# Kernel tuning notes

Hardware: AMD Instinct MI355X
Metric: run time of the kernel (lower is better)

Reference implementation:

```python
import jax, jax.numpy as jnp
import numpy as np

N_NODES = 100000
N_EDGES = 3200000
N_GRAPHS = 128


def setup_inputs() -> dict:
    key = jax.random.key(0)
    ks = jax.random.split(key, 16)
    x = jax.random.normal(ks[0], (N_NODES, 47), dtype=jnp.float32)
    edge_index = jax.random.randint(ks[1], (2, N_EDGES), 0, N_NODES, dtype=jnp.int32)
    batch = jnp.sort(jax.random.randint(ks[2], (N_NODES,), 0, N_GRAPHS, dtype=jnp.int32))

    def w(k, shape):
        fan_in = shape[0]
        return jax.random.normal(k, shape, dtype=jnp.float32) * (1.0 / np.sqrt(fan_in))

    return {
        "x": x, "edge_index": edge_index, "batch": batch,
        "W1": w(ks[3], (47, 64)), "b1": jnp.zeros((64,), jnp.float32),
        "W2": w(ks[4], (64, 32)), "b2": jnp.zeros((32,), jnp.float32),
        "A1": w(ks[5], (32, 32)), "c1": jnp.zeros((32,), jnp.float32),
        "A2": w(ks[6], (32, 16)), "c2": jnp.zeros((16,), jnp.float32),
        "A3": w(ks[7], (16, 8)),  "c3": jnp.zeros((8,), jnp.float32),
        "A4": w(ks[8], (8, 1)),   "c4": jnp.zeros((1,), jnp.float32),
    }


def _gcn_conv(x, W, b, src, dst):
    # PyG GCNConv: h = XW, then D^-1/2 (A+I) D^-1/2 aggregation, then + bias.
    h = x @ W  # [N, out]
    ones = jnp.ones(dst.shape[0], dtype=h.dtype)
    deg = jax.ops.segment_sum(ones, dst, num_segments=N_NODES)  # incl. self loops
    dinv = jnp.where(deg > 0, jax.lax.rsqrt(deg), 0.0)
    norm = dinv[src] * dinv[dst]  # [E_total]
    msg = h[src] * norm[:, None]  # gather + normalize
    out = jax.ops.segment_sum(msg, dst, num_segments=N_NODES)  # scatter-add
    return out + b


def reference(x, edge_index, batch, W1, b1, W2, b2, A1, c1, A2, c2, A3, c3, A4, c4):
    loops = jnp.arange(N_NODES, dtype=edge_index.dtype)
    src = jnp.concatenate([edge_index[0], loops])
    dst = jnp.concatenate([edge_index[1], loops])
    h = jax.nn.relu(_gcn_conv(x, W1, b1, src, dst))
    h = jax.nn.relu(_gcn_conv(h, W2, b2, src, dst))
    # dropout is identity in eval mode
    g = jax.ops.segment_sum(h, batch, num_segments=N_GRAPHS)  # global_add_pool [G,32]
    g = jax.nn.relu(g @ A1 + c1)
    g = jax.nn.relu(g @ A2 + c2)
    g = jax.nn.relu(g @ A3 + c3)
    return g @ A4 + c4  # [G, 1]
```

## Files before the change

kernel.cpp:

```cpp
#include <hip/hip_runtime.h>

#define N_NODES 100000
#define N_EDGES 3200000
#define N_GRAPHS 128

#define RSHIFT 8
#define NPR 256
#define R_RANGES ((N_NODES + NPR - 1) / NPR)
#define CAP 9472
#define C_CHUNKS 1024
#define EPC (N_EDGES / C_CHUNKS)
#define SRC_BITS 17

#define XPB 64
#define AXW 48

__device__ inline unsigned short f2bf(float f) {
    unsigned u = __float_as_uint(f);
    unsigned r = u + 0x7FFFu + ((u >> 16) & 1u);
    return (unsigned short)(r >> 16);
}
__device__ inline float bflo(unsigned u) { return __uint_as_float(u << 16); }
__device__ inline float bfhi(unsigned u) { return __uint_as_float(u & 0xFFFF0000u); }


__global__ __launch_bounds__(256) void padcvt_kernel(const float* __restrict__ x,
                                                     unsigned short* __restrict__ xpb,
                                                     int* __restrict__ range_next) {
    if (blockIdx.x < 2) {
        int i = blockIdx.x * 256 + threadIdx.x;
        if (i < R_RANGES) range_next[i] = i * CAP;
    }
    int idx = blockIdx.x * 256 + threadIdx.x;
    if (idx >= N_NODES * XPB) return;
    int n = idx >> 6;
    int c = idx & 63;
    float v = (c < 47) ? x[n * 47 + c] : 0.f;
    xpb[idx] = f2bf(v);
}


__global__ __launch_bounds__(256) void partition_kernel(const int* __restrict__ src,
                                                        const int* __restrict__ dst,
                                                        int* __restrict__ range_next,
                                                        int* __restrict__ bucket) {
    __shared__ int cntL[R_RANGES];
    __shared__ int baseL[R_RANGES];
    const int t = threadIdx.x, b = blockIdx.x;
    const int e0 = b * EPC, e1 = e0 + EPC;
    for (int i = t; i < R_RANGES; i += 256) cntL[i] = 0;
    __syncthreads();
    for (int e = e0 + t; e < e1; e += 256) atomicAdd(&cntL[dst[e] >> RSHIFT], 1);
    __syncthreads();
    for (int i = t; i < R_RANGES; i += 256) {
        int c = cntL[i];
        baseL[i] = (c > 0) ? atomicAdd(&range_next[i], c) : 0;
        cntL[i] = 0;
    }
    __syncthreads();
    for (int e = e0 + t; e < e1; e += 256) {
        int d = dst[e];
        int s = src[e];
        int r = d >> RSHIFT;
        int p = baseL[r] + atomicAdd(&cntL[r], 1);
        if (p < (r + 1) * CAP)
            bucket[p] = ((d & (NPR - 1)) << SRC_BITS) | s;
    }
}


__global__ __launch_bounds__(256) void build_kernel(const int* __restrict__ bucket,
                                                    const int* __restrict__ range_next,
                                                    int* __restrict__ row_ptr,
                                                    int* __restrict__ row_cnt,
                                                    float* __restrict__ dinv,
                                                    int* __restrict__ csr_src) {
    __shared__ int sE[CAP];
    __shared__ int degs[NPR];
    __shared__ int part[256];
    const int t = threadIdx.x, r = blockIdx.x;
    const int base_node = r * NPR;
    const int seg0 = r * CAP;
    int m = range_next[r] - seg0;
    if (m > CAP) m = CAP;
    for (int i = t; i < m; i += 256) sE[i] = bucket[seg0 + i];
    degs[t] = 0;
    __syncthreads();
    for (int i = t; i < m; i += 256) atomicAdd(&degs[sE[i] >> SRC_BITS], 1);
    __syncthreads();
    int d = degs[t];
    part[t] = d;
    __syncthreads();
    for (int dd = 1; dd < 256; dd <<= 1) {
        int tv = (t >= dd) ? part[t - dd] : 0;
        __syncthreads();
        part[t] += tv;
        __syncthreads();
    }
    int ex = part[t] - d;
    int node = base_node + t;
    if (node < N_NODES) {
        row_ptr[node] = seg0 + ex;
        row_cnt[node] = d;
        dinv[node] = rsqrtf((float)(d + 1));
    }
    degs[t] = ex;
    __syncthreads();
    for (int i = t; i < m; i += 256) {
        int p = sE[i];
        int pos = atomicAdd(&degs[p >> SRC_BITS], 1);
        csr_src[seg0 + pos] = p & ((1 << SRC_BITS) - 1);
    }
}


__global__ __launch_bounds__(256) void wprep_kernel(const int* __restrict__ csr_src,
                                                    const int* __restrict__ range_next,
                                                    const float* __restrict__ dinv,
                                                    float* __restrict__ csr_w) {
    const int t = threadIdx.x, r = blockIdx.x;
    const int seg0 = r * CAP;
    int m = range_next[r] - seg0;
    if (m > CAP) m = CAP;
    for (int i = t; i < m; i += 256) {
        csr_w[seg0 + i] = dinv[csr_src[seg0 + i]];
    }
}


__global__ __launch_bounds__(256) void aggX_kernel(const unsigned short* __restrict__ xpb,
                                                   const float* __restrict__ dinv,
                                                   const int* __restrict__ row_ptr,
                                                   const int* __restrict__ row_cnt,
                                                   const int* __restrict__ csr_src,
                                                   const float* __restrict__ csr_w,
                                                   unsigned short* __restrict__ aggxb) {
    const int tid = threadIdx.x;
    const int n = blockIdx.x * 4 + (tid >> 6);
    if (n >= N_NODES) return;
    const int l = tid & 63;
    const int eo = l >> 3;
    const int cg = l & 7;
    const float dn = dinv[n];

    float acc[8] = {0.f, 0.f, 0.f, 0.f, 0.f, 0.f, 0.f, 0.f};
    if (eo == 0) {
        uint4 q = *(const uint4*)(xpb + (size_t)n * XPB + cg * 8);
        float w = dn * dn;
        acc[0] = bflo(q.x) * w; acc[1] = bfhi(q.x) * w;
        acc[2] = bflo(q.y) * w; acc[3] = bfhi(q.y) * w;
        acc[4] = bflo(q.z) * w; acc[5] = bfhi(q.z) * w;
        acc[6] = bflo(q.w) * w; acc[7] = bfhi(q.w) * w;
    }
    const int st = row_ptr[n];
    const int cnt = row_cnt[n];
    int k = eo;
    for (; k + 8 < cnt; k += 16) {
        int s0 = csr_src[st + k];
        int s1 = csr_src[st + k + 8];
        float w0 = csr_w[st + k] * dn;
        float w1 = csr_w[st + k + 8] * dn;
        uint4 q0 = *(const uint4*)(xpb + (size_t)s0 * XPB + cg * 8);
        uint4 q1 = *(const uint4*)(xpb + (size_t)s1 * XPB + cg * 8);
        acc[0] = fmaf(bflo(q0.x), w0, acc[0]); acc[1] = fmaf(bfhi(q0.x), w0, acc[1]);
        acc[2] = fmaf(bflo(q0.y), w0, acc[2]); acc[3] = fmaf(bfhi(q0.y), w0, acc[3]);
        acc[4] = fmaf(bflo(q0.z), w0, acc[4]); acc[5] = fmaf(bfhi(q0.z), w0, acc[5]);
        acc[6] = fmaf(bflo(q0.w), w0, acc[6]); acc[7] = fmaf(bfhi(q0.w), w0, acc[7]);
        acc[0] = fmaf(bflo(q1.x), w1, acc[0]); acc[1] = fmaf(bfhi(q1.x), w1, acc[1]);
        acc[2] = fmaf(bflo(q1.y), w1, acc[2]); acc[3] = fmaf(bfhi(q1.y), w1, acc[3]);
        acc[4] = fmaf(bflo(q1.z), w1, acc[4]); acc[5] = fmaf(bfhi(q1.z), w1, acc[5]);
        acc[6] = fmaf(bflo(q1.w), w1, acc[6]); acc[7] = fmaf(bfhi(q1.w), w1, acc[7]);
    }
    if (k < cnt) {
        int s0 = csr_src[st + k];
        float w0 = csr_w[st + k] * dn;
        uint4 q0 = *(const uint4*)(xpb + (size_t)s0 * XPB + cg * 8);
        acc[0] = fmaf(bflo(q0.x), w0, acc[0]); acc[1] = fmaf(bfhi(q0.x), w0, acc[1]);
        acc[2] = fmaf(bflo(q0.y), w0, acc[2]); acc[3] = fmaf(bfhi(q0.y), w0, acc[3]);
        acc[4] = fmaf(bflo(q0.z), w0, acc[4]); acc[5] = fmaf(bfhi(q0.z), w0, acc[5]);
        acc[6] = fmaf(bflo(q0.w), w0, acc[6]); acc[7] = fmaf(bfhi(q0.w), w0, acc[7]);
    }
#pragma unroll
    for (int off = 8; off <= 32; off <<= 1) {
#pragma unroll
        for (int j = 0; j < 8; ++j) acc[j] += __shfl_xor(acc[j], off);
    }
    if (eo == 0 && cg < 6) {
        uint4 o;
        o.x = ((unsigned)f2bf(acc[1]) << 16) | f2bf(acc[0]);
        o.y = ((unsigned)f2bf(acc[3]) << 16) | f2bf(acc[2]);
        o.z = ((unsigned)f2bf(acc[5]) << 16) | f2bf(acc[4]);
        o.w = ((unsigned)f2bf(acc[7]) << 16) | f2bf(acc[6]);
        *(uint4*)(aggxb + (size_t)n * AXW + cg * 8) = o;
    }
}


#define FGW1 52
#define FGW2 68

__global__ __launch_bounds__(256) void fusedgemm_kernel(const unsigned short* __restrict__ aggxb,
                                                        const float* __restrict__ W1,
                                                        const float* __restrict__ b1,
                                                        const float* __restrict__ W2,
                                                        unsigned short* __restrict__ zb) {
    __shared__ float W1t[64 * FGW1];
    __shared__ float W2t[32 * FGW2];
    __shared__ float b1s[64];
    __shared__ float rows[4][4][48];
    __shared__ float ts[4][4][64];
    const int t = threadIdx.x;
    for (int i = t; i < 48 * 64; i += 256) { int k = i >> 6, c = i & 63; W1t[c * FGW1 + k] = W1[i]; }
    for (int i = t; i < 64 * 32; i += 256) { int k = i >> 5, c = i & 31; W2t[c * FGW2 + k] = W2[i]; }
    if (t < 64) b1s[t] = b1[t];
    __syncthreads();

    const int w = t >> 6, l = t & 63;
    const int nb0 = blockIdx.x * 64 + w * 16;
    const float* wc1 = &W1t[l * FGW1];
    const int nn = l >> 5, c2 = l & 31;
    const float* wc2 = &W2t[c2 * FGW2];

    for (int p = 0; p < 4; ++p) {
        const int n0 = nb0 + p * 4;
        if (n0 >= N_NODES) break;
        if (l < 48) {
#pragma unroll
            for (int j = 0; j < 4; ++j)
                rows[w][j][l] = bflo(aggxb[(size_t)(n0 + j) * AXW + l]);
        }
        {
            float h0 = b1s[l], h1 = h0, h2 = h0, h3 = h0;
#pragma unroll
            for (int k4 = 0; k4 < 48; k4 += 4) {
                float4 wv = *(const float4*)(wc1 + k4);
                float4 r0 = *(const float4*)&rows[w][0][k4];
                float4 r1 = *(const float4*)&rows[w][1][k4];
                float4 r2 = *(const float4*)&rows[w][2][k4];
                float4 r3 = *(const float4*)&rows[w][3][k4];
                h0 = fmaf(r0.x, wv.x, h0); h0 = fmaf(r0.y, wv.y, h0); h0 = fmaf(r0.z, wv.z, h0); h0 = fmaf(r0.w, wv.w, h0);
                h1 = fmaf(r1.x, wv.x, h1); h1 = fmaf(r1.y, wv.y, h1); h1 = fmaf(r1.z, wv.z, h1); h1 = fmaf(r1.w, wv.w, h1);
                h2 = fmaf(r2.x, wv.x, h2); h2 = fmaf(r2.y, wv.y, h2); h2 = fmaf(r2.z, wv.z, h2); h2 = fmaf(r2.w, wv.w, h2);
                h3 = fmaf(r3.x, wv.x, h3); h3 = fmaf(r3.y, wv.y, h3); h3 = fmaf(r3.z, wv.z, h3); h3 = fmaf(r3.w, wv.w, h3);
            }
            ts[w][0][l] = fmaxf(h0, 0.f);
            ts[w][1][l] = fmaxf(h1, 0.f);
            ts[w][2][l] = fmaxf(h2, 0.f);
            ts[w][3][l] = fmaxf(h3, 0.f);
        }
#pragma unroll
        for (int sp = 0; sp < 2; ++sp) {
            const float* tv = ts[w][sp * 2 + nn];
            float z = 0.f;
#pragma unroll
            for (int k4 = 0; k4 < 64; k4 += 4) {
                float4 a = *(const float4*)(tv + k4);
                float4 wv = *(const float4*)(wc2 + k4);
                z = fmaf(a.x, wv.x, z); z = fmaf(a.y, wv.y, z); z = fmaf(a.z, wv.z, z); z = fmaf(a.w, wv.w, z);
            }
            zb[(size_t)(n0 + sp * 2 + nn) * 32 + c2] = f2bf(z);
        }
    }
}


__global__ __launch_bounds__(256) void aggregate32_kernel(const unsigned short* __restrict__ zb,
                                                          const float* __restrict__ dinv,
                                                          const int* __restrict__ row_ptr,
                                                          const int* __restrict__ row_cnt,
                                                          const int* __restrict__ csr_src,
                                                          const float* __restrict__ csr_w,
                                                          const float* __restrict__ bias,
                                                          float* __restrict__ out) {
    const int tid = threadIdx.x;
    const int n = blockIdx.x * 4 + (tid >> 6);
    if (n >= N_NODES) return;
    const int l = tid & 63;
    const int eo = l >> 2;
    const int cg = l & 3;
    const float dn = dinv[n];

    float acc[8] = {0.f, 0.f, 0.f, 0.f, 0.f, 0.f, 0.f, 0.f};
    if (eo == 0) {
        uint4 q = *(const uint4*)(zb + (size_t)n * 32 + cg * 8);
        float w = dn * dn;
        acc[0] = bflo(q.x) * w; acc[1] = bfhi(q.x) * w;
        acc[2] = bflo(q.y) * w; acc[3] = bfhi(q.y) * w;
        acc[4] = bflo(q.z) * w; acc[5] = bfhi(q.z) * w;
        acc[6] = bflo(q.w) * w; acc[7] = bfhi(q.w) * w;
    }
    const int st = row_ptr[n];
    const int cnt = row_cnt[n];
    int k = eo;
    for (; k + 16 < cnt; k += 32) {
        int s0 = csr_src[st + k];
        int s1 = csr_src[st + k + 16];
        float w0 = csr_w[st + k] * dn;
        float w1 = csr_w[st + k + 16] * dn;
        uint4 q0 = *(const uint4*)(zb + (size_t)s0 * 32 + cg * 8);
        uint4 q1 = *(const uint4*)(zb + (size_t)s1 * 32 + cg * 8);
        acc[0] = fmaf(bflo(q0.x), w0, acc[0]); acc[1] = fmaf(bfhi(q0.x), w0, acc[1]);
        acc[2] = fmaf(bflo(q0.y), w0, acc[2]); acc[3] = fmaf(bfhi(q0.y), w0, acc[3]);
        acc[4] = fmaf(bflo(q0.z), w0, acc[4]); acc[5] = fmaf(bfhi(q0.z), w0, acc[5]);
        acc[6] = fmaf(bflo(q0.w), w0, acc[6]); acc[7] = fmaf(bfhi(q0.w), w0, acc[7]);
        acc[0] = fmaf(bflo(q1.x), w1, acc[0]); acc[1] = fmaf(bfhi(q1.x), w1, acc[1]);
        acc[2] = fmaf(bflo(q1.y), w1, acc[2]); acc[3] = fmaf(bfhi(q1.y), w1, acc[3]);
        acc[4] = fmaf(bflo(q1.z), w1, acc[4]); acc[5] = fmaf(bfhi(q1.z), w1, acc[5]);
        acc[6] = fmaf(bflo(q1.w), w1, acc[6]); acc[7] = fmaf(bfhi(q1.w), w1, acc[7]);
    }
    if (k < cnt) {
        int s0 = csr_src[st + k];
        float w0 = csr_w[st + k] * dn;
        uint4 q0 = *(const uint4*)(zb + (size_t)s0 * 32 + cg * 8);
        acc[0] = fmaf(bflo(q0.x), w0, acc[0]); acc[1] = fmaf(bfhi(q0.x), w0, acc[1]);
        acc[2] = fmaf(bflo(q0.y), w0, acc[2]); acc[3] = fmaf(bfhi(q0.y), w0, acc[3]);
        acc[4] = fmaf(bflo(q0.z), w0, acc[4]); acc[5] = fmaf(bfhi(q0.z), w0, acc[5]);
        acc[6] = fmaf(bflo(q0.w), w0, acc[6]); acc[7] = fmaf(bfhi(q0.w), w0, acc[7]);
    }
#pragma unroll
    for (int off = 4; off <= 32; off <<= 1) {
#pragma unroll
        for (int j = 0; j < 8; ++j) acc[j] += __shfl_xor(acc[j], off);
    }
    if (eo == 0) {
        const float* bp = bias + cg * 8;
        float4 a, b;
        a.x = fmaxf(acc[0] + bp[0], 0.f);
        a.y = fmaxf(acc[1] + bp[1], 0.f);
        a.z = fmaxf(acc[2] + bp[2], 0.f);
        a.w = fmaxf(acc[3] + bp[3], 0.f);
        b.x = fmaxf(acc[4] + bp[4], 0.f);
        b.y = fmaxf(acc[5] + bp[5], 0.f);
        b.z = fmaxf(acc[6] + bp[6], 0.f);
        b.w = fmaxf(acc[7] + bp[7], 0.f);
        *(float4*)(out + (size_t)n * 32 + cg * 8) = a;
        *(float4*)(out + (size_t)n * 32 + cg * 8 + 4) = b;
    }
}


#define POOL_NPB 256

__global__ __launch_bounds__(256) void pool_kernel(const int* __restrict__ batch,
                                                   const float* __restrict__ h,
                                                   float* __restrict__ g) {
    const int t = threadIdx.x;
    const int c = t & 31;
    const int r = t >> 5;
    int i0 = blockIdx.x * POOL_NPB;
    int i1 = i0 + POOL_NPB;
    if (i1 > N_NODES) i1 = N_NODES;
    int cur_g = -1;
    float acc = 0.f;
    for (int i = i0 + r; i < i1; i += 8) {
        int gi = batch[i];
        float v = h[(size_t)i * 32 + c];
        if (gi != cur_g) {
            if (cur_g >= 0) atomicAdd(&g[cur_g * 32 + c], acc);
            acc = 0.f;
            cur_g = gi;
        }
        acc += v;
    }
    if (cur_g >= 0) atomicAdd(&g[cur_g * 32 + c], acc);
}


__global__ __launch_bounds__(128) void mlp_kernel(const float* __restrict__ g,
                                                  const float* __restrict__ A1, const float* __restrict__ c1,
                                                  const float* __restrict__ A2, const float* __restrict__ c2,
                                                  const float* __restrict__ A3, const float* __restrict__ c3,
                                                  const float* __restrict__ A4, const float* __restrict__ c4,
                                                  float* __restrict__ out) {
    int t = threadIdx.x;
    float v[32];
#pragma unroll
    for (int k = 0; k < 32; ++k) v[k] = g[t * 32 + k];
    float u[32];
#pragma unroll
    for (int c = 0; c < 32; ++c) {
        float s = c1[c];
#pragma unroll
        for (int k = 0; k < 32; ++k) s = fmaf(v[k], A1[k * 32 + c], s);
        u[c] = fmaxf(s, 0.f);
    }
    float w[16];
#pragma unroll
    for (int c = 0; c < 16; ++c) {
        float s = c2[c];
#pragma unroll
        for (int k = 0; k < 32; ++k) s = fmaf(u[k], A2[k * 16 + c], s);
        w[c] = fmaxf(s, 0.f);
    }
    float z[8];
#pragma unroll
    for (int c = 0; c < 8; ++c) {
        float s = c3[c];
#pragma unroll
        for (int k = 0; k < 16; ++k) s = fmaf(w[k], A3[k * 8 + c], s);
        z[c] = fmaxf(s, 0.f);
    }
    float s = c4[0];
#pragma unroll
    for (int k = 0; k < 8; ++k) s = fmaf(z[k], A4[k], s);
    out[t] = s;
}


extern "C" void kernel_launch(void* const* d_in, const int* in_sizes, int n_in,
                              void* d_out, int out_size, void* d_ws, size_t ws_size,
                              hipStream_t stream) {
    const float* x    = (const float*)d_in[0];
    const int*   ei   = (const int*)d_in[1];
    const int*   srcE = ei;
    const int*   dstE = ei + N_EDGES;
    const int*   batch = (const int*)d_in[2];
    const float* W1 = (const float*)d_in[3];  const float* b1 = (const float*)d_in[4];
    const float* W2 = (const float*)d_in[5];  const float* b2 = (const float*)d_in[6];
    const float* A1 = (const float*)d_in[7];  const float* c1 = (const float*)d_in[8];
    const float* A2 = (const float*)d_in[9];  const float* c2 = (const float*)d_in[10];
    const float* A3 = (const float*)d_in[11]; const float* c3 = (const float*)d_in[12];
    const float* A4 = (const float*)d_in[13]; const float* c4 = (const float*)d_in[14];
    float* out = (float*)d_out;

    char* ws = (char*)d_ws;
    size_t off_b = 0;
    auto take = [&](size_t bytes) -> char* {
        char* p = ws + off_b;
        off_b = (off_b + bytes + 255) & ~(size_t)255;
        return p;
    };
    int*            row_ptr    = (int*)take((size_t)N_NODES * 4);
    int*            row_cnt    = (int*)take((size_t)N_NODES * 4);
    float*          dinv       = (float*)take((size_t)N_NODES * 4);
    int*            range_next = (int*)take((size_t)R_RANGES * 4);
    int*            csr_src    = (int*)take((size_t)R_RANGES * CAP * 4);
    float*          csr_w      = (float*)take((size_t)R_RANGES * CAP * 4);
    char*           bz_raw     = take((size_t)R_RANGES * CAP * 4);
    int*            bucket     = (int*)bz_raw;
    unsigned short* zb         = (unsigned short*)bz_raw;
    unsigned short* xpb        = (unsigned short*)take((size_t)N_NODES * XPB * 2);
    char*           aa_raw     = take((size_t)N_NODES * 32 * 4);
    unsigned short* aggxb      = (unsigned short*)aa_raw;
    float*          agg        = (float*)aa_raw;
    float*          g          = (float*)take((size_t)N_GRAPHS * 32 * 4);
    (void)ws_size; (void)in_sizes; (void)n_in; (void)out_size;

    padcvt_kernel<<<(N_NODES * XPB + 255) / 256, 256, 0, stream>>>(x, xpb, range_next);

    partition_kernel<<<C_CHUNKS, 256, 0, stream>>>(srcE, dstE, range_next, bucket);
    build_kernel<<<R_RANGES, 256, 0, stream>>>(bucket, range_next, row_ptr, row_cnt, dinv, csr_src);
    wprep_kernel<<<R_RANGES, 256, 0, stream>>>(csr_src, range_next, dinv, csr_w);

    aggX_kernel<<<(N_NODES + 3) / 4, 256, 0, stream>>>(xpb, dinv, row_ptr, row_cnt, csr_src, csr_w, aggxb);
    fusedgemm_kernel<<<(N_NODES + 63) / 64, 256, 0, stream>>>(aggxb, W1, b1, W2, zb);
    aggregate32_kernel<<<(N_NODES + 3) / 4, 256, 0, stream>>>(zb, dinv, row_ptr, row_cnt, csr_src, csr_w, b2, agg);

    hipMemsetAsync(g, 0, (size_t)N_GRAPHS * 32 * 4, stream);
    pool_kernel<<<(N_NODES + POOL_NPB - 1) / POOL_NPB, 256, 0, stream>>>(batch, agg, g);
    mlp_kernel<<<1, 128, 0, stream>>>(g, A1, c1, A2, c2, A3, c3, A4, c4, out);
}
```

Before: 398.6 us.

## Locally sort edges by range in LDS before writing partition buckets

```diff
diff --git a/kernel.cpp b/kernel.cpp
--- a/kernel.cpp
+++ b/kernel.cpp
@@ -8,7 +8,7 @@
 #define NPR 256
 #define R_RANGES ((N_NODES + NPR - 1) / NPR)
 #define CAP 9472
-#define C_CHUNKS 1024
+#define C_CHUNKS 512
 #define EPC (N_EDGES / C_CHUNKS)
 #define SRC_BITS 17
 
@@ -44,27 +44,54 @@
                                                         const int* __restrict__ dst,
                                                         int* __restrict__ range_next,
                                                         int* __restrict__ bucket) {
+    __shared__ int sorted[EPC];
+    __shared__ unsigned short rid[EPC];
     __shared__ int cntL[R_RANGES];
+    __shared__ int lstart[R_RANGES];
     __shared__ int baseL[R_RANGES];
+    __shared__ int scanbuf[256];
     const int t = threadIdx.x, b = blockIdx.x;
-    const int e0 = b * EPC, e1 = e0 + EPC;
+    const int e0 = b * EPC;
     for (int i = t; i < R_RANGES; i += 256) cntL[i] = 0;
     __syncthreads();
-    for (int e = e0 + t; e < e1; e += 256) atomicAdd(&cntL[dst[e] >> RSHIFT], 1);
-    __syncthreads();
-    for (int i = t; i < R_RANGES; i += 256) {
-        int c = cntL[i];
-        baseL[i] = (c > 0) ? atomicAdd(&range_next[i], c) : 0;
-        cntL[i] = 0;
-    }
-    __syncthreads();
-    for (int e = e0 + t; e < e1; e += 256) {
-        int d = dst[e];
-        int s = src[e];
+    for (int i = t; i < EPC; i += 256) atomicAdd(&cntL[dst[e0 + i] >> RSHIFT], 1);
+    __syncthreads();
+    int i0 = 2 * t, i1 = 2 * t + 1;
+    int v0 = (i0 < R_RANGES) ? cntL[i0] : 0;
+    int v1 = (i1 < R_RANGES) ? cntL[i1] : 0;
+    int s = v0 + v1;
+    scanbuf[t] = s;
+    __syncthreads();
+    for (int d = 1; d < 256; d <<= 1) {
+        int tv = (t >= d) ? scanbuf[t - d] : 0;
+        __syncthreads();
+        scanbuf[t] += tv;
+        __syncthreads();
+    }
+    int ex = scanbuf[t] - s;
+    if (i0 < R_RANGES) {
+        lstart[i0] = ex;
+        baseL[i0] = (v0 > 0) ? atomicAdd(&range_next[i0], v0) : 0;
+        cntL[i0] = 0;
+    }
+    if (i1 < R_RANGES) {
+        lstart[i1] = ex + v0;
+        baseL[i1] = (v1 > 0) ? atomicAdd(&range_next[i1], v1) : 0;
+        cntL[i1] = 0;
+    }
+    __syncthreads();
+    for (int i = t; i < EPC; i += 256) {
+        int d = dst[e0 + i];
+        int sv = src[e0 + i];
         int r = d >> RSHIFT;
-        int p = baseL[r] + atomicAdd(&cntL[r], 1);
-        if (p < (r + 1) * CAP)
-            bucket[p] = ((d & (NPR - 1)) << SRC_BITS) | s;
+        int q = lstart[r] + atomicAdd(&cntL[r], 1);
+        sorted[q] = ((d & (NPR - 1)) << SRC_BITS) | sv;
+        rid[q] = (unsigned short)r;
+    }
+    __syncthreads();
+    for (int i = t; i < EPC; i += 256) {
+        int r = rid[i];
+        bucket[baseL[r] + (i - lstart[r])] = sorted[i];
     }
 }
 
```

After: 385.2 us. 1.03x faster.
